# Kernel optimization log

Measured on AMD Instinct MI355X. Metric: run time of the kernel, lower is better.

Reference implementation:

```python
import jax, jax.numpy as jnp
import numpy as np

B, N, D, H = 4, 4096, 512, 512
EDGE_P = 0.01  # adjacency density


def _glorot(key, shape):
    fan_in, fan_out = shape
    limit = np.sqrt(6.0 / (fan_in + fan_out)).astype(np.float32)
    return jax.random.uniform(key, shape, jnp.float32, -limit, limit)


def setup_inputs() -> dict:
    key = jax.random.key(0)
    ks = jax.random.split(key, 9)
    batch_graph = jax.random.normal(ks[0], (B, N, D), jnp.float32)
    adj = (jax.random.uniform(ks[1], (B, N, N)) < EDGE_P).astype(jnp.float32)
    adj = jnp.minimum(adj + jnp.eye(N, dtype=jnp.float32)[None], 1.0)  # self loops, 0/1
    return {
        "batch_graph": batch_graph,
        "adj": adj,
        "W1": _glorot(ks[2], (D, H)), "b1": jnp.zeros((H,), jnp.float32),
        "W2": _glorot(ks[3], (H, H)), "b2": jnp.zeros((H,), jnp.float32),
        "W3": _glorot(ks[4], (H, D)), "b3": jnp.zeros((D,), jnp.float32),
    }


def _normalize_adj(adj):
    # Faithful to GCN.normalize_sparse_adj: D^{-1/2} A^T D^{-1/2}
    rowsum = adj.sum(axis=1)                       # [B, N] (sum over dim 1, as in torch)
    d_inv_sqrt = jnp.where(rowsum > 0, jax.lax.rsqrt(jnp.maximum(rowsum, 1e-30)), 0.0)
    # (A @ diag(d))^T @ diag(d)  ->  d_i * A[j,i] * d_j
    return d_inv_sqrt[:, :, None] * jnp.swapaxes(adj, 1, 2) * d_inv_sqrt[:, None, :]


def reference(batch_graph, adj, W1, b1, W2, b2, W3, b3):
    # Block-diagonal big_adj @ big_graph == independent per-batch matmuls;
    # we exploit that instead of materializing the [B*N, B*N] dense matrix.
    a = _normalize_adj(adj)                                   # [B, N, N]
    # GraphConvolution (pygcn-style): out = adj @ (x @ W) + b; dropout = identity (eval)
    h = jax.nn.relu(jnp.einsum('bij,bjd->bid', a, batch_graph @ W1) + b1)
    h = jax.nn.relu(jnp.einsum('bij,bjd->bid', a, h @ W2) + b2)
    out = jnp.einsum('bij,bjd->bid', a, h @ W3) + b3          # [B, N, D]
    return out
```

## Files before the change

### kernel.cpp

```cpp
#include <hip/hip_runtime.h>
#include <stdint.h>

#define CAP 128
#define RPB 4

typedef __attribute__((ext_vector_type(8))) short bf16x8;
typedef __attribute__((ext_vector_type(4))) float f32x4;

typedef __attribute__((address_space(3))) uint32_t lds_u32;
typedef __attribute__((address_space(1))) const uint32_t glb_u32;

__device__ __forceinline__ unsigned short f2bf(float f) {
  union { float f; uint32_t u; } c; c.f = f;
  return (unsigned short)((c.u + 0x7fffu + ((c.u >> 16) & 1u)) >> 16);
}
__device__ __forceinline__ float bf2f(uint32_t b) {
  union { uint32_t u; float f; } c; c.u = b << 16; return c.f;
}
__device__ __forceinline__ float as_f32(uint32_t u) {
  union { uint32_t u; float f; } c; c.u = u; return c.f;
}

__global__ __launch_bounds__(256) void k_detect(const uint32_t* __restrict__ a,
                                                int* __restrict__ flag) {
  int i = blockIdx.x * 256 + threadIdx.x;
  bool found = false;
  for (int k = 0; k < 64; k++) {
    uint32_t x = a[(size_t)k * 65536 + i];
    if (x == 0x00003F80u || x == 0x3F803F80u) found = true;
  }
  if (found) flag[0] = 1;
}

__global__ __launch_bounds__(256) void k_build(const void* __restrict__ adjp,
                                               int* __restrict__ cnt,
                                               int* __restrict__ cols,
                                               const int* __restrict__ flag) {
  int gid = blockIdx.x * 256 + threadIdx.x;
  if (flag[0]) {
    const uint4* a = (const uint4*)adjp;
    uint4 v = a[gid];
    int i0 = (gid & 511) * 8;
    int j  = (gid >> 9) & 4095;
    int b  = gid >> 21;
    int base = b << 12;
    uint32_t w[4] = {v.x, v.y, v.z, v.w};
#pragma unroll
    for (int q = 0; q < 4; q++) {
      if (w[q] & 0xffffu) {
        int c = base + i0 + q * 2;
        int p = atomicAdd(&cnt[c], 1);
        if (p < CAP) cols[((size_t)c << 7) + p] = j;
      }
      if (w[q] >> 16) {
        int c = base + i0 + q * 2 + 1;
        int p = atomicAdd(&cnt[c], 1);
        if (p < CAP) cols[((size_t)c << 7) + p] = j;
      }
    }
  } else {
    const float4* a = (const float4*)adjp;
#pragma unroll
    for (int it = 0; it < 2; it++) {
      int v4 = gid + it * 8388608;
      float4 v = a[v4];
      int i0 = (v4 & 1023) * 4;
      int j  = (v4 >> 10) & 4095;
      int b  = v4 >> 22;
      int base = b << 12;
      float e[4] = {v.x, v.y, v.z, v.w};
#pragma unroll
      for (int q = 0; q < 4; q++) {
        if (e[q] != 0.0f) {
          int c = base + i0 + q;
          int p = atomicAdd(&cnt[c], 1);
          if (p < CAP) cols[((size_t)c << 7) + p] = j;
        }
      }
    }
  }
}

__global__ __launch_bounds__(256) void k_post(const void* __restrict__ xp,
                                              ushort* __restrict__ xb,
                                              const void* w1, const void* w2,
                                              const void* w3,
                                              ushort* __restrict__ wt1,
                                              ushort* __restrict__ wt2,
                                              ushort* __restrict__ wt3,
                                              const int* __restrict__ cnt,
                                              float* __restrict__ dinv,
                                              const void* b1, const void* b2,
                                              const void* b3,
                                              float* __restrict__ b1f,
                                              float* __restrict__ b2f,
                                              float* __restrict__ b3f,
                                              const int* __restrict__ flag) {
  int B = blockIdx.x;
  int t = threadIdx.x;
  if (B < 4096) {
    if (flag[0]) return;
    int gid = B * 256 + t;
    const float4* in = (const float4*)xp;
#pragma unroll
    for (int it = 0; it < 2; it++) {
      int i = gid + it * 1048576;
      float4 v = in[i];
      uint32_t lo = (uint32_t)f2bf(v.x) | ((uint32_t)f2bf(v.y) << 16);
      uint32_t hi = (uint32_t)f2bf(v.z) | ((uint32_t)f2bf(v.w) << 16);
      ((uint2*)xb)[i] = make_uint2(lo, hi);
    }
  } else if (B < 7168) {
    int id = (B - 4096) * 256 + t;
    int w = id >> 18;
    int o = id & 262143;
    const void* wp = (w == 0) ? w1 : (w == 1) ? w2 : w3;
    ushort* wt = (w == 0) ? wt1 : (w == 1) ? wt2 : wt3;
    int n = o >> 9, k = o & 511;
    if (flag[0]) wt[o] = ((const ushort*)wp)[k * 512 + n];
    else         wt[o] = f2bf(((const float*)wp)[k * 512 + n]);
  } else {
    int id = (B - 7168) * 256 + t;
    if (id < 16384) {
      int c = cnt[id];
      dinv[id] = (c > 0) ? 1.0f / sqrtf((float)c) : 0.0f;
    } else {
      int o = id - 16384;
      if (o < 1536) {
        const void* src = (o < 512) ? b1 : (o < 1024) ? b2 : b3;
        float* dst = (o < 512) ? b1f : (o < 1024) ? b2f : b3f;
        int i = o & 511;
        dst[i] = flag[0] ? bf2f(((const ushort*)src)[i]) : ((const float*)src)[i];
      }
    }
  }
}

__device__ __forceinline__ void gl_lds16(const ushort* g, ushort* l) {
  __builtin_amdgcn_global_load_lds((glb_u32*)g, (lds_u32*)l, 16, 0, 0);
}

__global__ __launch_bounds__(256) void k_gemm(const void* __restrict__ Xraw,
                                              const ushort* __restrict__ Xconv,
                                              const ushort* __restrict__ WT,
                                              ushort* __restrict__ Z,
                                              const int* __restrict__ flag) {
  __shared__ ushort As[128 * 32];
  __shared__ ushort Bs[128 * 32];
  const int K = 512, NO = 512;
  const ushort* X = flag[0] ? (const ushort*)Xraw : Xconv;
  int tid = threadIdx.x;
  int m0 = blockIdx.y * 128, n0 = blockIdx.x * 128;
  int lane = tid & 63;
  int wv = tid >> 6;
  int wm = (wv >> 1) << 6;
  int wn = (wv & 1) << 6;
  int lr = lane & 15;
  int lq = lane >> 4;

  f32x4 zero = {0.f, 0.f, 0.f, 0.f};
  f32x4 acc[4][4];
#pragma unroll
  for (int im = 0; im < 4; im++)
#pragma unroll
    for (int in_ = 0; in_ < 4; in_++) acc[im][in_] = zero;

  const ushort* Xg = X  + (size_t)(m0 + (tid >> 2)) * K + ((tid & 3) << 3);
  const ushort* Wg = WT + (size_t)(n0 + (tid >> 2)) * K + ((tid & 3) << 3);

  for (int kt = 0; kt < K; kt += 32) {
    __syncthreads();
    gl_lds16(Xg + kt,                    &As[tid * 8]);
    gl_lds16(Xg + kt + (size_t)64 * K,   &As[2048 + tid * 8]);
    gl_lds16(Wg + kt,                    &Bs[tid * 8]);
    gl_lds16(Wg + kt + (size_t)64 * K,   &Bs[2048 + tid * 8]);
    __syncthreads();
    bf16x8 af[4], bfr[4];
#pragma unroll
    for (int im = 0; im < 4; im++)
      af[im] = *(const bf16x8*)&As[(wm + im * 16 + lr) * 32 + lq * 8];
#pragma unroll
    for (int in_ = 0; in_ < 4; in_++)
      bfr[in_] = *(const bf16x8*)&Bs[(wn + in_ * 16 + lr) * 32 + lq * 8];
#pragma unroll
    for (int im = 0; im < 4; im++)
#pragma unroll
      for (int in_ = 0; in_ < 4; in_++)
        acc[im][in_] = __builtin_amdgcn_mfma_f32_16x16x32_bf16(
            af[im], bfr[in_], acc[im][in_], 0, 0, 0);
  }

#pragma unroll
  for (int im = 0; im < 4; im++) {
    int row0 = m0 + wm + im * 16 + lq * 4;
#pragma unroll
    for (int in_ = 0; in_ < 4; in_++) {
      int col = n0 + wn + in_ * 16 + lr;
#pragma unroll
      for (int r = 0; r < 4; r++)
        Z[(size_t)(row0 + r) * NO + col] = f2bf(acc[im][in_][r]);
    }
  }
}

__global__ __launch_bounds__(256) void k_spmm(const ushort* __restrict__ Z,
                                              const int* __restrict__ cnt,
                                              const int* __restrict__ cols,
                                              const float* __restrict__ dinv,
                                              const float* __restrict__ bias,
                                              void* __restrict__ outp,
                                              int do_relu, int is_final,
                                              const int* __restrict__ flag,
                                              int pass) {
  __shared__ int   sj[RPB][CAP];
  __shared__ float sv[RPB][CAP];
  int B = blockIdx.x;
  int wv = threadIdx.x >> 6;
  int lane = threadIdx.x & 63;
  int r = B * RPB + wv;
  int base = (r >> 12) << 12;

  int nnz = cnt[r];
  if (nnz > CAP) nnz = CAP;
  float dr = dinv[r];
  for (int k = lane; k < nnz; k += 64) {
    int j = cols[((size_t)r << 7) + k];
    sj[wv][k] = j;
    sv[wv][k] = dr * dinv[base + j];
  }

  int g = lane >> 4;
  int col = (lane & 15) << 3;
  const ushort* Zc = Z + (size_t)base * 512 + pass * 128 + col;

  float a[8] = {0.f, 0.f, 0.f, 0.f, 0.f, 0.f, 0.f, 0.f};
  for (int k = 0; k < nnz; k += 4) {
    int e = k + g;
    bool ok = e < nnz;
    int   j = ok ? sj[wv][e] : 0;
    float v = ok ? sv[wv][e] : 0.f;
    uint4 z = *(const uint4*)(Zc + (size_t)j * 512);
    uint32_t w[4] = {z.x, z.y, z.z, z.w};
#pragma unroll
    for (int q = 0; q < 4; q++) {
      a[q * 2]     += v * as_f32(w[q] << 16);
      a[q * 2 + 1] += v * as_f32(w[q] & 0xffff0000u);
    }
  }

#pragma unroll
  for (int q = 0; q < 8; q++) {
    a[q] += __shfl_xor(a[q], 16);
    a[q] += __shfl_xor(a[q], 32);
  }
  if (lane >= 16) return;

  const float4* bp = (const float4*)(bias + pass * 128 + col);
  float4 bb0 = bp[0], bb1 = bp[1];
  float bv[8] = {bb0.x, bb0.y, bb0.z, bb0.w, bb1.x, bb1.y, bb1.z, bb1.w};
#pragma unroll
  for (int q = 0; q < 8; q++) {
    a[q] += bv[q];
    if (do_relu) a[q] = fmaxf(a[q], 0.f);
  }

  if (!is_final || flag[0]) {
    uint4 o;
    o.x = (uint32_t)f2bf(a[0]) | ((uint32_t)f2bf(a[1]) << 16);
    o.y = (uint32_t)f2bf(a[2]) | ((uint32_t)f2bf(a[3]) << 16);
    o.z = (uint32_t)f2bf(a[4]) | ((uint32_t)f2bf(a[5]) << 16);
    o.w = (uint32_t)f2bf(a[6]) | ((uint32_t)f2bf(a[7]) << 16);
    *(uint4*)((ushort*)outp + (size_t)r * 512 + pass * 128 + col) = o;
  } else {
    float4* op = (float4*)((float*)outp + (size_t)r * 512 + pass * 128 + col);
    op[0] = make_float4(a[0], a[1], a[2], a[3]);
    op[1] = make_float4(a[4], a[5], a[6], a[7]);
  }
}

extern "C" void kernel_launch(void* const* d_in, const int* in_sizes, int n_in,
                              void* d_out, int out_size, void* d_ws, size_t ws_size,
                              hipStream_t stream) {
  const void* X  = d_in[0];
  const void* A  = d_in[1];
  const void* W1 = d_in[2]; const void* b1 = d_in[3];
  const void* W2 = d_in[4]; const void* b2 = d_in[5];
  const void* W3 = d_in[6]; const void* b3 = d_in[7];

  char* ws = (char*)d_ws;
  size_t off = 0;
  auto alloc = [&](size_t bytes) -> void* {
    void* p = ws + off;
    off += (bytes + 255) & ~(size_t)255;
    return p;
  };
  int*    cnt  = (int*)alloc(16384 * 4);
  int*    flag = (int*)alloc(4);
  float*  dinv = (float*)alloc(16384 * 4);
  int*    cols = (int*)alloc((size_t)16384 * CAP * 4);
  ushort* W1T  = (ushort*)alloc(512 * 512 * 2);
  ushort* W2T  = (ushort*)alloc(512 * 512 * 2);
  ushort* W3T  = (ushort*)alloc(512 * 512 * 2);
  float*  b1f  = (float*)alloc(512 * 4);
  float*  b2f  = (float*)alloc(512 * 4);
  float*  b3f  = (float*)alloc(512 * 4);
  ushort* Xb   = (ushort*)alloc((size_t)16384 * 512 * 2);
  ushort* Zb   = (ushort*)alloc((size_t)16384 * 512 * 2);
  ushort* Hb   = (ushort*)alloc((size_t)16384 * 512 * 2);

  hipMemsetAsync(cnt, 0, 65536 + 256, stream);

  k_detect<<<256, 256, 0, stream>>>((const uint32_t*)A, flag);
  k_build<<<32768, 256, 0, stream>>>(A, cnt, cols, flag);
  k_post<<<7238, 256, 0, stream>>>(X, Xb, W1, W2, W3, W1T, W2T, W3T,
                                   cnt, dinv, b1, b2, b3, b1f, b2f, b3f, flag);

  dim3 gg(4, 128);
  k_gemm<<<gg, 256, 0, stream>>>(X, Xb, W1T, Zb, flag);
  for (int p = 0; p < 4; p++)
    k_spmm<<<4096, 256, 0, stream>>>(Zb, cnt, cols, dinv, b1f, Hb, 1, 0, flag, p);
  k_gemm<<<gg, 256, 0, stream>>>(Hb, Hb, W2T, Zb, flag);
  for (int p = 0; p < 4; p++)
    k_spmm<<<4096, 256, 0, stream>>>(Zb, cnt, cols, dinv, b2f, Xb, 1, 0, flag, p);
  k_gemm<<<gg, 256, 0, stream>>>(Xb, Xb, W3T, Zb, flag);
  for (int p = 0; p < 4; p++)
    k_spmm<<<4096, 256, 0, stream>>>(Zb, cnt, cols, dinv, b3f, d_out, 0, 1, flag, p);
}
```

Measured before the change: 699.6 us.

## Rewrite SpMM as persistent XCC-affine work-stealing kernel covering full row width

The four column-pass SpMM launches per layer become one persistent launch of 512 blocks. Each wave now covers all 512 columns of a row, and blocks pull row chunks from per-batch atomic queues, starting at a batch chosen from the hardware XCC id so that each XCC's L2 holds a single batch's Z matrix. The inner loop is unrolled by two edges, bias is folded into the accumulator initialisation, and adjacency reads, cols reads and outputs use nontemporal loads and stores. This removes the repeated gather setup and redundant column-index traffic across passes, in exchange for atomic queue overhead and two block-wide barriers per chunk.

```diff
diff --git a/kernel.cpp b/kernel.cpp
--- a/kernel.cpp
+++ b/kernel.cpp
@@ -6,9 +6,12 @@
 
 typedef __attribute__((ext_vector_type(8))) short bf16x8;
 typedef __attribute__((ext_vector_type(4))) float f32x4;
+typedef __attribute__((ext_vector_type(4))) uint32_t u32x4;
 
 typedef __attribute__((address_space(3))) uint32_t lds_u32;
 typedef __attribute__((address_space(1))) const uint32_t glb_u32;
+
+#define GETREG_XCC ((31 << 11) | (0 << 6) | 20)
 
 __device__ __forceinline__ unsigned short f2bf(float f) {
   union { float f; uint32_t u; } c; c.f = f;
@@ -38,8 +41,8 @@
                                                const int* __restrict__ flag) {
   int gid = blockIdx.x * 256 + threadIdx.x;
   if (flag[0]) {
-    const uint4* a = (const uint4*)adjp;
-    uint4 v = a[gid];
+    const u32x4* a = (const u32x4*)adjp;
+    u32x4 v = __builtin_nontemporal_load(&a[gid]);
     int i0 = (gid & 511) * 8;
     int j  = (gid >> 9) & 4095;
     int b  = gid >> 21;
@@ -59,11 +62,11 @@
       }
     }
   } else {
-    const float4* a = (const float4*)adjp;
+    const f32x4* a = (const f32x4*)adjp;
 #pragma unroll
     for (int it = 0; it < 2; it++) {
       int v4 = gid + it * 8388608;
-      float4 v = a[v4];
+      f32x4 v = __builtin_nontemporal_load(&a[v4]);
       int i0 = (v4 & 1023) * 4;
       int j  = (v4 >> 10) & 4095;
       int b  = v4 >> 22;
@@ -211,70 +214,88 @@
                                               void* __restrict__ outp,
                                               int do_relu, int is_final,
                                               const int* __restrict__ flag,
-                                              int pass) {
+                                              int* __restrict__ q) {
   __shared__ int   sj[RPB][CAP];
   __shared__ float sv[RPB][CAP];
-  int B = blockIdx.x;
+  __shared__ int s_chunk;
   int wv = threadIdx.x >> 6;
   int lane = threadIdx.x & 63;
-  int r = B * RPB + wv;
-  int base = (r >> 12) << 12;
-
-  int nnz = cnt[r];
-  if (nnz > CAP) nnz = CAP;
-  float dr = dinv[r];
-  for (int k = lane; k < nnz; k += 64) {
-    int j = cols[((size_t)r << 7) + k];
-    sj[wv][k] = j;
-    sv[wv][k] = dr * dinv[base + j];
-  }
-
-  int g = lane >> 4;
-  int col = (lane & 15) << 3;
-  const ushort* Zc = Z + (size_t)base * 512 + pass * 128 + col;
-
-  float a[8] = {0.f, 0.f, 0.f, 0.f, 0.f, 0.f, 0.f, 0.f};
-  for (int k = 0; k < nnz; k += 4) {
-    int e = k + g;
-    bool ok = e < nnz;
-    int   j = ok ? sj[wv][e] : 0;
-    float v = ok ? sv[wv][e] : 0.f;
-    uint4 z = *(const uint4*)(Zc + (size_t)j * 512);
-    uint32_t w[4] = {z.x, z.y, z.z, z.w};
-#pragma unroll
-    for (int q = 0; q < 4; q++) {
-      a[q * 2]     += v * as_f32(w[q] << 16);
-      a[q * 2 + 1] += v * as_f32(w[q] & 0xffff0000u);
-    }
-  }
-
-#pragma unroll
-  for (int q = 0; q < 8; q++) {
-    a[q] += __shfl_xor(a[q], 16);
-    a[q] += __shfl_xor(a[q], 32);
-  }
-  if (lane >= 16) return;
-
-  const float4* bp = (const float4*)(bias + pass * 128 + col);
+  int pref = (__builtin_amdgcn_s_getreg(GETREG_XCC) & 7) >> 1;
+
+  const float4* bp = (const float4*)bias + lane * 2;
   float4 bb0 = bp[0], bb1 = bp[1];
-  float bv[8] = {bb0.x, bb0.y, bb0.z, bb0.w, bb1.x, bb1.y, bb1.z, bb1.w};
-#pragma unroll
-  for (int q = 0; q < 8; q++) {
-    a[q] += bv[q];
-    if (do_relu) a[q] = fmaxf(a[q], 0.f);
-  }
-
-  if (!is_final || flag[0]) {
-    uint4 o;
-    o.x = (uint32_t)f2bf(a[0]) | ((uint32_t)f2bf(a[1]) << 16);
-    o.y = (uint32_t)f2bf(a[2]) | ((uint32_t)f2bf(a[3]) << 16);
-    o.z = (uint32_t)f2bf(a[4]) | ((uint32_t)f2bf(a[5]) << 16);
-    o.w = (uint32_t)f2bf(a[6]) | ((uint32_t)f2bf(a[7]) << 16);
-    *(uint4*)((ushort*)outp + (size_t)r * 512 + pass * 128 + col) = o;
-  } else {
-    float4* op = (float4*)((float*)outp + (size_t)r * 512 + pass * 128 + col);
-    op[0] = make_float4(a[0], a[1], a[2], a[3]);
-    op[1] = make_float4(a[4], a[5], a[6], a[7]);
+
+  for (int attempt = 0; attempt < 4; attempt++) {
+    int b = (pref + attempt) & 3;
+    int base = b << 12;
+    const ushort* Zb = Z + (size_t)base * 512 + lane * 8;
+    while (true) {
+      __syncthreads();
+      if (threadIdx.x == 0) s_chunk = atomicAdd(&q[b], 1);
+      __syncthreads();
+      int chunk = s_chunk;
+      if (chunk >= 1024) break;
+      int r = base + chunk * RPB + wv;
+
+      int nnz = cnt[r];
+      if (nnz > CAP) nnz = CAP;
+      float dr = dinv[r];
+      for (int k = lane; k < nnz; k += 64) {
+        int j = __builtin_nontemporal_load(&cols[((size_t)r << 7) + k]);
+        sj[wv][k] = j;
+        sv[wv][k] = dr * dinv[base + j];
+      }
+
+      float a[8] = {bb0.x, bb0.y, bb0.z, bb0.w, bb1.x, bb1.y, bb1.z, bb1.w};
+      int k = 0;
+      for (; k + 2 <= nnz; k += 2) {
+        int j0 = sj[wv][k], j1 = sj[wv][k + 1];
+        float v0 = sv[wv][k], v1 = sv[wv][k + 1];
+        u32x4 z0 = *(const u32x4*)(Zb + (size_t)j0 * 512);
+        u32x4 z1 = *(const u32x4*)(Zb + (size_t)j1 * 512);
+        uint32_t w0[4] = {z0.x, z0.y, z0.z, z0.w};
+        uint32_t w1[4] = {z1.x, z1.y, z1.z, z1.w};
+#pragma unroll
+        for (int qq = 0; qq < 4; qq++) {
+          a[qq * 2]     += v0 * as_f32(w0[qq] << 16);
+          a[qq * 2 + 1] += v0 * as_f32(w0[qq] & 0xffff0000u);
+          a[qq * 2]     += v1 * as_f32(w1[qq] << 16);
+          a[qq * 2 + 1] += v1 * as_f32(w1[qq] & 0xffff0000u);
+        }
+      }
+      if (k < nnz) {
+        int j0 = sj[wv][k];
+        float v0 = sv[wv][k];
+        u32x4 z0 = *(const u32x4*)(Zb + (size_t)j0 * 512);
+        uint32_t w0[4] = {z0.x, z0.y, z0.z, z0.w};
+#pragma unroll
+        for (int qq = 0; qq < 4; qq++) {
+          a[qq * 2]     += v0 * as_f32(w0[qq] << 16);
+          a[qq * 2 + 1] += v0 * as_f32(w0[qq] & 0xffff0000u);
+        }
+      }
+
+      if (do_relu) {
+#pragma unroll
+        for (int qq = 0; qq < 8; qq++) a[qq] = fmaxf(a[qq], 0.f);
+      }
+
+      if (!is_final || flag[0]) {
+        u32x4 o;
+        o.x = (uint32_t)f2bf(a[0]) | ((uint32_t)f2bf(a[1]) << 16);
+        o.y = (uint32_t)f2bf(a[2]) | ((uint32_t)f2bf(a[3]) << 16);
+        o.z = (uint32_t)f2bf(a[4]) | ((uint32_t)f2bf(a[5]) << 16);
+        o.w = (uint32_t)f2bf(a[6]) | ((uint32_t)f2bf(a[7]) << 16);
+        __builtin_nontemporal_store(
+            o, (u32x4*)((ushort*)outp + (size_t)r * 512 + lane * 8));
+      } else {
+        f32x4* op = (f32x4*)((float*)outp + (size_t)r * 512 + lane * 8);
+        f32x4 o0 = {a[0], a[1], a[2], a[3]};
+        f32x4 o1 = {a[4], a[5], a[6], a[7]};
+        __builtin_nontemporal_store(o0, op);
+        __builtin_nontemporal_store(o1, op + 1);
+      }
+    }
   }
 }
 
@@ -296,6 +317,7 @@
   };
   int*    cnt  = (int*)alloc(16384 * 4);
   int*    flag = (int*)alloc(4);
+  int*    qs   = (int*)alloc(12 * 4);
   float*  dinv = (float*)alloc(16384 * 4);
   int*    cols = (int*)alloc((size_t)16384 * CAP * 4);
   ushort* W1T  = (ushort*)alloc(512 * 512 * 2);
@@ -308,7 +330,7 @@
   ushort* Zb   = (ushort*)alloc((size_t)16384 * 512 * 2);
   ushort* Hb   = (ushort*)alloc((size_t)16384 * 512 * 2);
 
-  hipMemsetAsync(cnt, 0, 65536 + 256, stream);
+  (void)hipMemsetAsync(cnt, 0, 65536 + 512, stream);
 
   k_detect<<<256, 256, 0, stream>>>((const uint32_t*)A, flag);
   k_build<<<32768, 256, 0, stream>>>(A, cnt, cols, flag);
@@ -317,12 +339,9 @@
 
   dim3 gg(4, 128);
   k_gemm<<<gg, 256, 0, stream>>>(X, Xb, W1T, Zb, flag);
-  for (int p = 0; p < 4; p++)
-    k_spmm<<<4096, 256, 0, stream>>>(Zb, cnt, cols, dinv, b1f, Hb, 1, 0, flag, p);
+  k_spmm<<<512, 256, 0, stream>>>(Zb, cnt, cols, dinv, b1f, Hb, 1, 0, flag, qs);
   k_gemm<<<gg, 256, 0, stream>>>(Hb, Hb, W2T, Zb, flag);
-  for (int p = 0; p < 4; p++)
-    k_spmm<<<4096, 256, 0, stream>>>(Zb, cnt, cols, dinv, b2f, Xb, 1, 0, flag, p);
+  k_spmm<<<512, 256, 0, stream>>>(Zb, cnt, cols, dinv, b2f, Xb, 1, 0, flag, qs + 4);
   k_gemm<<<gg, 256, 0, stream>>>(Xb, Xb, W3T, Zb, flag);
-  for (int p = 0; p < 4; p++)
-    k_spmm<<<4096, 256, 0, stream>>>(Zb, cnt, cols, dinv, b3f, d_out, 0, 1, flag, p);
-}
+  k_spmm<<<512, 256, 0, stream>>>(Zb, cnt, cols, dinv, b3f, d_out, 0, 1, flag, qs + 8);
+}
```

Result: slower. 788.9 us (+12.8%).
